# Performance work log

Measured on AMD Instinct MI355X. Metric: run time of the kernel, lower is better.

Reference implementation:

```python
import jax, jax.numpy as jnp
import numpy as np
import math

IN_DIM = 128
OUT_DIM = 128
EDGE_DIM = 16
LN_EPS = 1e-5


def setup_inputs() -> dict:
    key = jax.random.key(0)
    ks = jax.random.split(key, 6)
    bs, N = 8, 512
    x = jax.random.normal(ks[0], (bs, N, IN_DIM), dtype=jnp.float32)
    edge_feats = jax.random.normal(ks[1], (bs, N, N, EDGE_DIM), dtype=jnp.float32)
    # fc weight (out_dim, in_dim), xavier-uniform scale
    lim_w = math.sqrt(6.0 / (IN_DIM + OUT_DIM))
    W = jax.random.uniform(ks[2], (OUT_DIM, IN_DIM), minval=-lim_w, maxval=lim_w, dtype=jnp.float32)
    # attn_fc weight (1, 2*out_dim+edge_dim) split into a_src | a_dst | a_e
    fan_in = 2 * OUT_DIM + EDGE_DIM
    lim_a = math.sqrt(6.0 / (fan_in + 1))
    a = jax.random.uniform(ks[3], (fan_in,), minval=-lim_a, maxval=lim_a, dtype=jnp.float32)
    a_src, a_dst, a_e = a[:OUT_DIM], a[OUT_DIM:2 * OUT_DIM], a[2 * OUT_DIM:]
    gamma = jnp.ones((OUT_DIM,), dtype=jnp.float32)
    beta = jnp.zeros((OUT_DIM,), dtype=jnp.float32)
    return {"x": x, "edge_feats": edge_feats, "W": W, "a_src": a_src,
            "a_dst": a_dst, "a_e": a_e, "gamma": gamma, "beta": beta}


def reference(x, edge_feats, W, a_src, a_dst, a_e, gamma, beta):
    # h: (bs, N, out_dim)
    h = jnp.einsum('bni,oi->bno', x, W)
    scale = 1.0 / math.sqrt(OUT_DIM)
    # Decomposed rank-1 attention score: attn_fc([h_i, h_j, e_ij]) =
    # h_i.a_src + h_j.a_dst + e_ij.a_e  -- identical math, no (bs,N,N,2D+E) tensor.
    s_i = jnp.einsum('bnd,d->bn', h, a_src)           # row term (index i)
    s_j = jnp.einsum('bnd,d->bn', h, a_dst)           # col term (index j)
    s_e = jnp.einsum('bije,e->bij', edge_feats, a_e)  # edge term
    e_ij = (s_i[:, :, None] + s_j[:, None, :] + s_e) * scale  # (bs, N, N)
    # max-subtract then softmax over j (jax.nn.softmax is already max-stable,
    # and softmax(e - max) == softmax(e))
    alpha = jax.nn.softmax(e_ij, axis=-1)
    # weighted sum over neighbors j (dropout skipped: eval mode)
    h_prime = jnp.einsum('bij,bjd->bid', alpha, h)
    # LayerNorm over last dim
    mu = jnp.mean(h_prime, axis=-1, keepdims=True)
    var = jnp.var(h_prime, axis=-1, keepdims=True)
    out = (h_prime - mu) * jax.lax.rsqrt(var + LN_EPS) * gamma + beta
    return out
```

## Files before the change

### kernel.cpp

```cpp
#include <hip/hip_runtime.h>
#include <math.h>

#define NB 8
#define NN 512
#define D 128
#define TIF 4
#define JC 64
#define NCK (NN / JC)
#define K1R 8
#define LN_EPS 1e-5f
#define SCALE 0.08838834764831845f

typedef float f32x4 __attribute__((ext_vector_type(4)));

__device__ __forceinline__ float dotv(f32x4 a, f32x4 b) {
    f32x4 m = a * b;
    return m.x + m.y + m.z + m.w;
}
__device__ __forceinline__ float dot4(float4 a, float4 b) {
    return a.x * b.x + a.y * b.y + a.z * b.z + a.w * b.w;
}

__global__ __launch_bounds__(256) void k1_proj(
    const float* __restrict__ x, const float* __restrict__ W,
    const float* __restrict__ a_src, const float* __restrict__ a_dst,
    float* __restrict__ h_ws, float* __restrict__ si_ws, float* __restrict__ sj_ws)
{
    __shared__ __align__(16) float4 Wl[128][32];
    __shared__ __align__(16) float4 xl[K1R][32];
    __shared__ float redk[K1R][2][2];

    const int t = threadIdx.x;
    const int row0 = blockIdx.x * K1R;

    const float4* Wg = (const float4*)W;
#pragma unroll
    for (int k = 0; k < 16; ++k) {
        const int f = t + 256 * k;
        const int o = f >> 5, q = f & 31;
        Wl[o][q ^ (o & 7)] = Wg[f];
    }
    xl[t >> 5][t & 31] = ((const float4*)(x + (size_t)row0 * D))[t];
    __syncthreads();

    const int o = t & 127;
    const int rb = (t >> 7) * (K1R / 2);
    float acc[K1R / 2] = {0.f, 0.f, 0.f, 0.f};
#pragma unroll
    for (int q = 0; q < 32; ++q) {
        const float4 wv = Wl[o][q ^ (o & 7)];
#pragma unroll
        for (int r = 0; r < K1R / 2; ++r) acc[r] += dot4(wv, xl[rb + r][q]);
    }
    const float as = a_src[o], ad = a_dst[o];
#pragma unroll
    for (int r = 0; r < K1R / 2; ++r) {
        h_ws[(size_t)(row0 + rb + r) * D + o] = acc[r];
        float vs = acc[r] * as, vd = acc[r] * ad;
#pragma unroll
        for (int m = 32; m >= 1; m >>= 1) {
            vs += __shfl_xor(vs, m);
            vd += __shfl_xor(vd, m);
        }
        if ((t & 63) == 0) {
            redk[rb + r][0][(t >> 6) & 1] = vs;
            redk[rb + r][1][(t >> 6) & 1] = vd;
        }
    }
    __syncthreads();
    if (t < K1R) si_ws[row0 + t] = redk[t][0][0] + redk[t][0][1];
    else if (t < 2 * K1R) {
        const int r = t - K1R;
        sj_ws[row0 + r] = redk[r][1][0] + redk[r][1][1];
    }
}

__global__ __launch_bounds__(256, 4) void kfused(
    const float* __restrict__ ef, const float* __restrict__ a_e,
    const float* __restrict__ gamma, const float* __restrict__ beta,
    const float* __restrict__ h_ws,
    const float* __restrict__ sj_ws, float* __restrict__ out)
{
    __shared__ float sj_l[NN];
    __shared__ __align__(16) float ab[JC][TIF];
    __shared__ __align__(16) float part[4][TIF][D];
    __shared__ __align__(16) float lw[4][TIF];

    const int t = threadIdx.x;
    const int w = t >> 6;
    const int lane = t & 63;
    const int bid = blockIdx.x;
    const int b = bid >> 7;
    const int i0 = (bid & 127) * TIF;

    sj_l[t] = sj_ws[b * NN + t];
    sj_l[t + 256] = sj_ws[b * NN + t + 256];

    const int c = t & 3;
    const f32x4 A = ((const f32x4*)a_e)[c];
    const f32x4* ef4 = (const f32x4*)ef + ((size_t)b * NN + i0) * NN * 4;

    const int jl = t >> 2;
    const int dl = (t & 31) << 2;
    const int g = t >> 5;
    const float* hb = h_ws + (size_t)b * NN * D;

    f32x4 acc0 = {0.f, 0.f, 0.f, 0.f};
    f32x4 acc1 = {0.f, 0.f, 0.f, 0.f};
    f32x4 acc2 = {0.f, 0.f, 0.f, 0.f};
    f32x4 acc3 = {0.f, 0.f, 0.f, 0.f};
    f32x4 lp   = {0.f, 0.f, 0.f, 0.f};

    f32x4 p0 = ef4[0 * 2048 + t];
    f32x4 p1 = ef4[1 * 2048 + t];
    f32x4 p2 = ef4[2 * 2048 + t];
    f32x4 p3 = ef4[3 * 2048 + t];

    __syncthreads();

#pragma unroll 1
    for (int ck = 0; ck < NCK; ++ck) {
        {
            float d0 = dotv(p0, A), d1 = dotv(p1, A);
            float d2 = dotv(p2, A), d3 = dotv(p3, A);
            d0 += __shfl_xor(d0, 1); d0 += __shfl_xor(d0, 2);
            d1 += __shfl_xor(d1, 1); d1 += __shfl_xor(d1, 2);
            d2 += __shfl_xor(d2, 1); d2 += __shfl_xor(d2, 2);
            d3 += __shfl_xor(d3, 1); d3 += __shfl_xor(d3, 2);
            const float dsel = (c == 0) ? d0 : (c == 1) ? d1 : (c == 2) ? d2 : d3;
            const float al = __expf((sj_l[ck * JC + jl] + dsel) * SCALE);
            ab[jl][c] = al;
        }

        const int jl0 = g << 3;
        const int jg0 = ck * JC + jl0;
        const f32x4 hv0 = *(const f32x4*)(hb + (size_t)(jg0 + 0) * D + dl);
        const f32x4 hv1 = *(const f32x4*)(hb + (size_t)(jg0 + 1) * D + dl);
        const f32x4 hv2 = *(const f32x4*)(hb + (size_t)(jg0 + 2) * D + dl);
        const f32x4 hv3 = *(const f32x4*)(hb + (size_t)(jg0 + 3) * D + dl);
        const f32x4 hv4 = *(const f32x4*)(hb + (size_t)(jg0 + 4) * D + dl);
        const f32x4 hv5 = *(const f32x4*)(hb + (size_t)(jg0 + 5) * D + dl);
        const f32x4 hv6 = *(const f32x4*)(hb + (size_t)(jg0 + 6) * D + dl);
        const f32x4 hv7 = *(const f32x4*)(hb + (size_t)(jg0 + 7) * D + dl);
        __builtin_amdgcn_sched_barrier(0);

        if (ck + 1 < NCK) {
            const int off = (ck + 1) * 256 + t;
            p0 = ef4[0 * 2048 + off];
            p1 = ef4[1 * 2048 + off];
            p2 = ef4[2 * 2048 + off];
            p3 = ef4[3 * 2048 + off];
        }
        __builtin_amdgcn_sched_barrier(0);

        {
            const float* abp = &ab[0][0];
            const f32x4 a0v = *(const f32x4*)(abp + (jl0 + 0) * TIF);
            const f32x4 a1v = *(const f32x4*)(abp + (jl0 + 1) * TIF);
            const f32x4 a2v = *(const f32x4*)(abp + (jl0 + 2) * TIF);
            const f32x4 a3v = *(const f32x4*)(abp + (jl0 + 3) * TIF);
            const f32x4 a4v = *(const f32x4*)(abp + (jl0 + 4) * TIF);
            const f32x4 a5v = *(const f32x4*)(abp + (jl0 + 5) * TIF);
            const f32x4 a6v = *(const f32x4*)(abp + (jl0 + 6) * TIF);
            const f32x4 a7v = *(const f32x4*)(abp + (jl0 + 7) * TIF);
            acc0 += hv0 * a0v.x + hv1 * a1v.x + hv2 * a2v.x + hv3 * a3v.x
                  + hv4 * a4v.x + hv5 * a5v.x + hv6 * a6v.x + hv7 * a7v.x;
            acc1 += hv0 * a0v.y + hv1 * a1v.y + hv2 * a2v.y + hv3 * a3v.y
                  + hv4 * a4v.y + hv5 * a5v.y + hv6 * a6v.y + hv7 * a7v.y;
            acc2 += hv0 * a0v.z + hv1 * a1v.z + hv2 * a2v.z + hv3 * a3v.z
                  + hv4 * a4v.z + hv5 * a5v.z + hv6 * a6v.z + hv7 * a7v.z;
            acc3 += hv0 * a0v.w + hv1 * a1v.w + hv2 * a2v.w + hv3 * a3v.w
                  + hv4 * a4v.w + hv5 * a5v.w + hv6 * a6v.w + hv7 * a7v.w;
            lp += a0v + a1v + a2v + a3v + a4v + a5v + a6v + a7v;
        }
    }

#pragma unroll
    for (int cc = 0; cc < 4; ++cc) {
        acc0[cc] += __shfl_xor(acc0[cc], 32);
        acc1[cc] += __shfl_xor(acc1[cc], 32);
        acc2[cc] += __shfl_xor(acc2[cc], 32);
        acc3[cc] += __shfl_xor(acc3[cc], 32);
        lp[cc]   += __shfl_xor(lp[cc], 32);
    }
    if (lane < 32) {
        *(f32x4*)&part[w][0][dl] = acc0;
        *(f32x4*)&part[w][1][dl] = acc1;
        *(f32x4*)&part[w][2][dl] = acc2;
        *(f32x4*)&part[w][3][dl] = acc3;
    }
    if (lane == 0) *(f32x4*)&lw[w][0] = lp;
    __syncthreads();

    {
        const float l_r = lw[0][w] + lw[1][w] + lw[2][w] + lw[3][w];
        const float inv = 1.0f / l_r;
        const int d0 = lane, d1 = lane + 64;
        float v0 = 0.f, v1 = 0.f;
#pragma unroll
        for (int pw = 0; pw < 4; ++pw) {
            v0 += part[pw][w][d0];
            v1 += part[pw][w][d1];
        }
        v0 *= inv; v1 *= inv;
        float s = v0 + v1, qq = v0 * v0 + v1 * v1;
#pragma unroll
        for (int mm = 32; mm >= 1; mm >>= 1) {
            s += __shfl_xor(s, mm);
            qq += __shfl_xor(qq, mm);
        }
        const float mu = s * (1.f / 128.f);
        const float var = qq * (1.f / 128.f) - mu * mu;
        const float rs = rsqrtf(var + LN_EPS);
        const size_t ob = ((size_t)(b * NN + i0 + w)) * D;
        out[ob + d0] = (v0 - mu) * rs * gamma[d0] + beta[d0];
        out[ob + d1] = (v1 - mu) * rs * gamma[d1] + beta[d1];
    }
}

extern "C" void kernel_launch(void* const* d_in, const int* in_sizes, int n_in,
                              void* d_out, int out_size, void* d_ws, size_t ws_size,
                              hipStream_t stream) {
    const float* x     = (const float*)d_in[0];
    const float* ef    = (const float*)d_in[1];
    const float* W     = (const float*)d_in[2];
    const float* a_src = (const float*)d_in[3];
    const float* a_dst = (const float*)d_in[4];
    const float* a_e   = (const float*)d_in[5];
    const float* gamma = (const float*)d_in[6];
    const float* beta  = (const float*)d_in[7];
    float* out = (float*)d_out;

    float* h_ws  = (float*)d_ws;
    float* si_ws = h_ws + (size_t)NB * NN * D;
    float* sj_ws = si_ws + NB * NN;

    k1_proj<<<NB * NN / K1R, 256, 0, stream>>>(x, W, a_src, a_dst, h_ws, si_ws, sj_ws);
    kfused<<<NB * NN / TIF, 256, 0, stream>>>(ef, a_e, gamma, beta,
                                              h_ws, sj_ws, out);
}
```

Baseline: 48.33 us.

## Eliminate projection kernel by reassociating W through attention aggregation

Removes the separate projection kernel and the h workspace. Each block folds W^T·a_dst into a vector and computes the column scores as x·v. It aggregates raw x rows with the softmax weights and applies W to the four aggregated rows before LayerNorm. This saves one launch and the global write and read of h. In exchange every block recomputes the W^T·a_dst vector and 512 dot products of length 128 over x, which adds redundant work per block.

New measurement: 82.04 us. 69.7% more time.

```diff
diff --git a/kernel.cpp b/kernel.cpp
--- a/kernel.cpp
+++ b/kernel.cpp
@@ -7,7 +7,6 @@
 #define TIF 4
 #define JC 64
 #define NCK (NN / JC)
-#define K1R 8
 #define LN_EPS 1e-5f
 #define SCALE 0.08838834764831845f
 
@@ -17,74 +16,20 @@
     f32x4 m = a * b;
     return m.x + m.y + m.z + m.w;
 }
-__device__ __forceinline__ float dot4(float4 a, float4 b) {
-    return a.x * b.x + a.y * b.y + a.z * b.z + a.w * b.w;
-}
-
-__global__ __launch_bounds__(256) void k1_proj(
+
+__global__ __launch_bounds__(256, 4) void kall(
+    const float* __restrict__ ef, const float* __restrict__ a_e,
     const float* __restrict__ x, const float* __restrict__ W,
-    const float* __restrict__ a_src, const float* __restrict__ a_dst,
-    float* __restrict__ h_ws, float* __restrict__ si_ws, float* __restrict__ sj_ws)
-{
-    __shared__ __align__(16) float4 Wl[128][32];
-    __shared__ __align__(16) float4 xl[K1R][32];
-    __shared__ float redk[K1R][2][2];
-
-    const int t = threadIdx.x;
-    const int row0 = blockIdx.x * K1R;
-
-    const float4* Wg = (const float4*)W;
-#pragma unroll
-    for (int k = 0; k < 16; ++k) {
-        const int f = t + 256 * k;
-        const int o = f >> 5, q = f & 31;
-        Wl[o][q ^ (o & 7)] = Wg[f];
-    }
-    xl[t >> 5][t & 31] = ((const float4*)(x + (size_t)row0 * D))[t];
-    __syncthreads();
-
-    const int o = t & 127;
-    const int rb = (t >> 7) * (K1R / 2);
-    float acc[K1R / 2] = {0.f, 0.f, 0.f, 0.f};
-#pragma unroll
-    for (int q = 0; q < 32; ++q) {
-        const float4 wv = Wl[o][q ^ (o & 7)];
-#pragma unroll
-        for (int r = 0; r < K1R / 2; ++r) acc[r] += dot4(wv, xl[rb + r][q]);
-    }
-    const float as = a_src[o], ad = a_dst[o];
-#pragma unroll
-    for (int r = 0; r < K1R / 2; ++r) {
-        h_ws[(size_t)(row0 + rb + r) * D + o] = acc[r];
-        float vs = acc[r] * as, vd = acc[r] * ad;
-#pragma unroll
-        for (int m = 32; m >= 1; m >>= 1) {
-            vs += __shfl_xor(vs, m);
-            vd += __shfl_xor(vd, m);
-        }
-        if ((t & 63) == 0) {
-            redk[rb + r][0][(t >> 6) & 1] = vs;
-            redk[rb + r][1][(t >> 6) & 1] = vd;
-        }
-    }
-    __syncthreads();
-    if (t < K1R) si_ws[row0 + t] = redk[t][0][0] + redk[t][0][1];
-    else if (t < 2 * K1R) {
-        const int r = t - K1R;
-        sj_ws[row0 + r] = redk[r][1][0] + redk[r][1][1];
-    }
-}
-
-__global__ __launch_bounds__(256, 4) void kfused(
-    const float* __restrict__ ef, const float* __restrict__ a_e,
+    const float* __restrict__ a_dst,
     const float* __restrict__ gamma, const float* __restrict__ beta,
-    const float* __restrict__ h_ws,
-    const float* __restrict__ sj_ws, float* __restrict__ out)
+    float* __restrict__ out)
 {
     __shared__ float sj_l[NN];
     __shared__ __align__(16) float ab[JC][TIF];
     __shared__ __align__(16) float part[4][TIF][D];
     __shared__ __align__(16) float lw[4][TIF];
+    __shared__ __align__(16) float vdst[D];
+    __shared__ __align__(16) float yrow[TIF][D];
 
     const int t = threadIdx.x;
     const int w = t >> 6;
@@ -93,30 +38,55 @@
     const int b = bid >> 7;
     const int i0 = (bid & 127) * TIF;
 
-    sj_l[t] = sj_ws[b * NN + t];
-    sj_l[t + 256] = sj_ws[b * NN + t + 256];
+    const f32x4* ef4 = (const f32x4*)ef + ((size_t)b * NN + i0) * NN * 4;
+    f32x4 p0 = ef4[0 * 2048 + t];
+    f32x4 p1 = ef4[1 * 2048 + t];
+    f32x4 p2 = ef4[2 * 2048 + t];
+    f32x4 p3 = ef4[3 * 2048 + t];
+    __builtin_amdgcn_sched_barrier(0);
+
+    if (t < D) {
+        float v0 = 0.f, v1 = 0.f, v2 = 0.f, v3 = 0.f;
+#pragma unroll 8
+        for (int o = 0; o < D; o += 4) {
+            v0 += a_dst[o + 0] * W[(size_t)(o + 0) * D + t];
+            v1 += a_dst[o + 1] * W[(size_t)(o + 1) * D + t];
+            v2 += a_dst[o + 2] * W[(size_t)(o + 2) * D + t];
+            v3 += a_dst[o + 3] * W[(size_t)(o + 3) * D + t];
+        }
+        vdst[t] = (v0 + v1) + (v2 + v3);
+    }
+    __syncthreads();
+
+    const float* xb = x + (size_t)b * NN * D;
+    {
+        const f32x4* vd4 = (const f32x4*)vdst;
+#pragma unroll
+        for (int rep = 0; rep < 2; ++rep) {
+            const int jj = t + rep * 256;
+            const f32x4* xr = (const f32x4*)(xb + (size_t)jj * D);
+            float s0 = 0.f, s1 = 0.f;
+#pragma unroll 8
+            for (int k = 0; k < 32; k += 2) {
+                s0 += dotv(xr[k], vd4[k]);
+                s1 += dotv(xr[k + 1], vd4[k + 1]);
+            }
+            sj_l[jj] = s0 + s1;
+        }
+    }
+    __syncthreads();
 
     const int c = t & 3;
     const f32x4 A = ((const f32x4*)a_e)[c];
-    const f32x4* ef4 = (const f32x4*)ef + ((size_t)b * NN + i0) * NN * 4;
-
     const int jl = t >> 2;
     const int dl = (t & 31) << 2;
     const int g = t >> 5;
-    const float* hb = h_ws + (size_t)b * NN * D;
 
     f32x4 acc0 = {0.f, 0.f, 0.f, 0.f};
     f32x4 acc1 = {0.f, 0.f, 0.f, 0.f};
     f32x4 acc2 = {0.f, 0.f, 0.f, 0.f};
     f32x4 acc3 = {0.f, 0.f, 0.f, 0.f};
     f32x4 lp   = {0.f, 0.f, 0.f, 0.f};
-
-    f32x4 p0 = ef4[0 * 2048 + t];
-    f32x4 p1 = ef4[1 * 2048 + t];
-    f32x4 p2 = ef4[2 * 2048 + t];
-    f32x4 p3 = ef4[3 * 2048 + t];
-
-    __syncthreads();
 
 #pragma unroll 1
     for (int ck = 0; ck < NCK; ++ck) {
@@ -134,14 +104,14 @@
 
         const int jl0 = g << 3;
         const int jg0 = ck * JC + jl0;
-        const f32x4 hv0 = *(const f32x4*)(hb + (size_t)(jg0 + 0) * D + dl);
-        const f32x4 hv1 = *(const f32x4*)(hb + (size_t)(jg0 + 1) * D + dl);
-        const f32x4 hv2 = *(const f32x4*)(hb + (size_t)(jg0 + 2) * D + dl);
-        const f32x4 hv3 = *(const f32x4*)(hb + (size_t)(jg0 + 3) * D + dl);
-        const f32x4 hv4 = *(const f32x4*)(hb + (size_t)(jg0 + 4) * D + dl);
-        const f32x4 hv5 = *(const f32x4*)(hb + (size_t)(jg0 + 5) * D + dl);
-        const f32x4 hv6 = *(const f32x4*)(hb + (size_t)(jg0 + 6) * D + dl);
-        const f32x4 hv7 = *(const f32x4*)(hb + (size_t)(jg0 + 7) * D + dl);
+        const f32x4 hv0 = *(const f32x4*)(xb + (size_t)(jg0 + 0) * D + dl);
+        const f32x4 hv1 = *(const f32x4*)(xb + (size_t)(jg0 + 1) * D + dl);
+        const f32x4 hv2 = *(const f32x4*)(xb + (size_t)(jg0 + 2) * D + dl);
+        const f32x4 hv3 = *(const f32x4*)(xb + (size_t)(jg0 + 3) * D + dl);
+        const f32x4 hv4 = *(const f32x4*)(xb + (size_t)(jg0 + 4) * D + dl);
+        const f32x4 hv5 = *(const f32x4*)(xb + (size_t)(jg0 + 5) * D + dl);
+        const f32x4 hv6 = *(const f32x4*)(xb + (size_t)(jg0 + 6) * D + dl);
+        const f32x4 hv7 = *(const f32x4*)(xb + (size_t)(jg0 + 7) * D + dl);
         __builtin_amdgcn_sched_barrier(0);
 
         if (ck + 1 < NCK) {
@@ -202,8 +172,27 @@
             v0 += part[pw][w][d0];
             v1 += part[pw][w][d1];
         }
-        v0 *= inv; v1 *= inv;
-        float s = v0 + v1, qq = v0 * v0 + v1 * v1;
+        yrow[w][d0] = v0 * inv;
+        yrow[w][d1] = v1 * inv;
+    }
+    __syncthreads();
+
+    {
+        const int d0 = lane, d1 = lane + 64;
+        const f32x4* yv  = (const f32x4*)yrow[w];
+        const f32x4* Wd0 = (const f32x4*)(W + (size_t)d0 * D);
+        const f32x4* Wd1 = (const f32x4*)(W + (size_t)d1 * D);
+        float h0a = 0.f, h0b = 0.f, h1a = 0.f, h1b = 0.f;
+#pragma unroll 8
+        for (int k = 0; k < 32; k += 2) {
+            const f32x4 y0 = yv[k], y1 = yv[k + 1];
+            h0a += dotv(y0, Wd0[k]);
+            h0b += dotv(y1, Wd0[k + 1]);
+            h1a += dotv(y0, Wd1[k]);
+            h1b += dotv(y1, Wd1[k + 1]);
+        }
+        const float h0 = h0a + h0b, h1 = h1a + h1b;
+        float s = h0 + h1, qq = h0 * h0 + h1 * h1;
 #pragma unroll
         for (int mm = 32; mm >= 1; mm >>= 1) {
             s += __shfl_xor(s, mm);
@@ -213,8 +202,8 @@
         const float var = qq * (1.f / 128.f) - mu * mu;
         const float rs = rsqrtf(var + LN_EPS);
         const size_t ob = ((size_t)(b * NN + i0 + w)) * D;
-        out[ob + d0] = (v0 - mu) * rs * gamma[d0] + beta[d0];
-        out[ob + d1] = (v1 - mu) * rs * gamma[d1] + beta[d1];
+        out[ob + d0] = (h0 - mu) * rs * gamma[d0] + beta[d0];
+        out[ob + d1] = (h1 - mu) * rs * gamma[d1] + beta[d1];
     }
 }
 
@@ -224,18 +213,12 @@
     const float* x     = (const float*)d_in[0];
     const float* ef    = (const float*)d_in[1];
     const float* W     = (const float*)d_in[2];
-    const float* a_src = (const float*)d_in[3];
     const float* a_dst = (const float*)d_in[4];
     const float* a_e   = (const float*)d_in[5];
     const float* gamma = (const float*)d_in[6];
     const float* beta  = (const float*)d_in[7];
     float* out = (float*)d_out;
 
-    float* h_ws  = (float*)d_ws;
-    float* si_ws = h_ws + (size_t)NB * NN * D;
-    float* sj_ws = si_ws + NB * NN;
-
-    k1_proj<<<NB * NN / K1R, 256, 0, stream>>>(x, W, a_src, a_dst, h_ws, si_ws, sj_ws);
-    kfused<<<NB * NN / TIF, 256, 0, stream>>>(ef, a_e, gamma, beta,
-                                              h_ws, sj_ws, out);
+    kall<<<NB * NN / TIF, 256, 0, stream>>>(ef, a_e, x, W, a_dst,
+                                            gamma, beta, out);
 }
```
